# Kernel optimization log

Measured on AMD Instinct MI355X. Metric: run time of the kernel, lower is better.

Reference implementation:

```python
import jax, jax.numpy as jnp
import numpy as np

RADIUS = 1.0
NSAMPLE = 32


def _query_ball(new_xyz, xyz, radius, nsample):
    # new_xyz (B,M,3), xyz (B,N,3) -> idx (B,M,nsample) int32
    B, M, _ = new_xyz.shape
    N = xyz.shape[1]
    # squared distances via ||q||^2 + ||p||^2 - 2 q.p (avoids BxMxNx3 diff tensor)
    q2 = jnp.sum(new_xyz * new_xyz, axis=-1)          # (B,M)
    p2 = jnp.sum(xyz * xyz, axis=-1)                  # (B,N)
    qp = jnp.einsum('bmd,bnd->bmn', new_xyz, xyz)     # (B,M,N)
    dist2 = q2[:, :, None] + p2[:, None, :] - 2.0 * qp
    mask = dist2 < radius * radius
    ar = jnp.arange(N, dtype=jnp.int32)
    masked = jnp.where(mask, ar[None, None, :], jnp.int32(N + 1))  # (B,M,N)
    first = jnp.sort(masked, axis=2)[:, :, :nsample]               # (B,M,S)
    first_valid = first[:, :, :1]                                   # pad with first neighbor
    idx = jnp.where(first == N + 1, first_valid, first)
    return idx.astype(jnp.int32)


def _group(points, idx):
    # points (B,C,N), idx (B,M,S) -> (B,C,M,S) gather along N
    B, C, N = points.shape
    M, S = idx.shape[1], idx.shape[2]
    ie = jnp.broadcast_to(idx.reshape(B, 1, M * S).astype(jnp.int32), (B, C, M * S))
    return jnp.take_along_axis(points, ie, axis=2).reshape(B, C, M, S)


def setup_inputs() -> dict:
    key = jax.random.key(0)
    k1, k2 = jax.random.split(key)
    B, N, M, C = 8, 8192, 2048, 64
    xyz = jax.random.normal(k1, (B, N, 3), dtype=jnp.float32)
    # centroids are a subset of the cloud -> every ball query has >= 1 valid neighbor
    new_xyz = xyz[:, :M, :]
    features = jax.random.normal(k2, (B, C, N), dtype=jnp.float32)
    return {"xyz": xyz, "new_xyz": new_xyz, "features": features}


def reference(xyz, new_xyz, features):
    idx = _query_ball(new_xyz, xyz, RADIUS, NSAMPLE)                      # (B,M,S)
    grouped_xyz = _group(jnp.swapaxes(xyz, 1, 2), idx)                    # (B,3,M,S)
    grouped_xyz = grouped_xyz - jnp.swapaxes(new_xyz, 1, 2)[..., None]    # recenter
    grouped_feat = _group(features, idx)                                  # (B,C,M,S)
    return jnp.concatenate([grouped_xyz, grouped_feat], axis=1)           # (B,3+C,M,S)
```

## Files before the change

kernel.cpp:

```cpp
#include <hip/hip_runtime.h>

#define N_PTS 8192
#define M_Q   2048
#define C_F   64
#define NS    32
#define B_SZ  8


__global__ __launch_bounds__(256) void prep_kernel(
    const float* __restrict__ xyz, const float* __restrict__ nxyz,
    float4* __restrict__ xyz4, float* __restrict__ xyzT,
    float* __restrict__ nxyzT)
{
#pragma clang fp contract(off)
    const int i = blockIdx.x * 256 + (int)threadIdx.x;
    if (i < B_SZ * N_PTS) {
        const float p0 = xyz[i * 3 + 0];
        const float p1 = xyz[i * 3 + 1];
        const float p2 = xyz[i * 3 + 2];
        const float s  = (p0 * p0 + p1 * p1) + p2 * p2;
        xyz4[i] = make_float4(p0, p1, p2, s);
        const int b = i >> 13;
        const int n = i & (N_PTS - 1);
        xyzT[((size_t)b * 3 + 0) * N_PTS + n] = p0;
        xyzT[((size_t)b * 3 + 1) * N_PTS + n] = p1;
        xyzT[((size_t)b * 3 + 2) * N_PTS + n] = p2;
    } else {
        const int j = i - B_SZ * N_PTS;
        const float q0 = nxyz[j * 3 + 0];
        const float q1 = nxyz[j * 3 + 1];
        const float q2 = nxyz[j * 3 + 2];
        const int b = j >> 11;
        const int m = j & (M_Q - 1);
        nxyzT[((size_t)b * 3 + 0) * M_Q + m] = q0;
        nxyzT[((size_t)b * 3 + 1) * M_Q + m] = q1;
        nxyzT[((size_t)b * 3 + 2) * M_Q + m] = q2;
    }
}

__global__ __launch_bounds__(256) void scan_kernel(
    const float4* __restrict__ xyz4, const float* __restrict__ nxyz,
    int* __restrict__ gidx)
{
#pragma clang fp contract(off)
    const int lane = threadIdx.x & 63;
    const int w    = threadIdx.x >> 6;
    const int q    = blockIdx.x * 4 + w;
    const int b    = q >> 11;
    const float4* __restrict__ xb = xyz4 + (size_t)b * N_PTS;
    int* __restrict__ gout = gidx + (size_t)q * NS;

    const float* __restrict__ qp = nxyz + (size_t)q * 3;
    const float qx = qp[0], qy = qp[1], qz = qp[2];
    const float q2 = (qx * qx + qy * qy) + qz * qz;

    int  cnt = 0;
    int  first_idx = 0;
    bool have_first = false;

    for (int base = 0; base < N_PTS && cnt < NS; base += 256) {
        float4 P[4];
#pragma unroll
        for (int cc = 0; cc < 4; ++cc)
            P[cc] = xb[base + cc * 64 + lane];
#pragma unroll
        for (int cc = 0; cc < 4; ++cc) {
            if (cnt >= NS) break;
            const float qpdot = (qx * P[cc].x + qy * P[cc].y) + qz * P[cc].z;
            const float d2 = (q2 + P[cc].w) - 2.0f * qpdot;
            const bool pred = d2 < 1.0f;
            const unsigned long long mask = __ballot(pred);
            if (mask) {
                if (!have_first) {
                    first_idx = base + cc * 64 + __ffsll(mask) - 1;
                    have_first = true;
                }
                if (pred) {
                    const int pos = cnt + (int)__popcll(mask & ((1ull << lane) - 1ull));
                    if (pos < NS) gout[pos] = base + cc * 64 + lane;
                }
                cnt += (int)__popcll(mask);
            }
        }
    }
    if (cnt < NS) {
        for (int p = cnt + lane; p < NS; p += 64) gout[p] = first_idx;
    }
}

__global__ __launch_bounds__(256) void gather_kernel(
    const float* __restrict__ feat, const float* __restrict__ xyzT,
    const float* __restrict__ nxyzT, const int* __restrict__ gidx,
    float* __restrict__ out)
{
#pragma clang fp contract(off)
    __shared__ float plane[N_PTS];
    __shared__ float qsh[512];

    const int x   = blockIdx.x & 7;
    const int t   = blockIdx.x >> 3;
    const int gq  = t / 67;
    const int c   = t % 67;
    const int gid = gq * 8 + x;
    const int b   = gid >> 2;
    const int mq  = gid & 3;
    const int m0  = mq * 512;

    const float* __restrict__ src =
        (c < 3) ? (xyzT + ((size_t)b * 3 + c) * N_PTS)
                : (feat + ((size_t)b * C_F + (c - 3)) * N_PTS);

    {
        const float4* __restrict__ s4 = (const float4*)src;
        float4* p4 = (float4*)plane;
#pragma unroll
        for (int k = 0; k < 8; ++k)
            p4[k * 256 + threadIdx.x] = s4[k * 256 + threadIdx.x];
    }
    if (c < 3) {
        const float* __restrict__ qsrc = nxyzT + ((size_t)b * 3 + c) * M_Q + m0;
        qsh[threadIdx.x]       = qsrc[threadIdx.x];
        qsh[256 + threadIdx.x] = qsrc[256 + threadIdx.x];
    }
    __syncthreads();

    const int* __restrict__ idxp = gidx + ((size_t)b * M_Q + m0) * NS;
    float* __restrict__ op = out + (((size_t)b * 67 + c) * M_Q + m0) * NS;

    if (c < 3) {
#pragma unroll 4
        for (int it = 0; it < 16; ++it) {
            const int e  = it * 256 + (int)threadIdx.x;
            const int m  = e >> 3;
            const int s4 = (e & 7) * 4;
            const int4 nn = *(const int4*)(idxp + m * NS + s4);
            const float qc = qsh[m];
            float4 v;
            v.x = plane[nn.x] - qc;
            v.y = plane[nn.y] - qc;
            v.z = plane[nn.z] - qc;
            v.w = plane[nn.w] - qc;
            *(float4*)(op + (size_t)m * NS + s4) = v;
        }
    } else {
#pragma unroll 4
        for (int it = 0; it < 16; ++it) {
            const int e  = it * 256 + (int)threadIdx.x;
            const int m  = e >> 3;
            const int s4 = (e & 7) * 4;
            const int4 nn = *(const int4*)(idxp + m * NS + s4);
            float4 v;
            v.x = plane[nn.x];
            v.y = plane[nn.y];
            v.z = plane[nn.z];
            v.w = plane[nn.w];
            *(float4*)(op + (size_t)m * NS + s4) = v;
        }
    }
}

extern "C" void kernel_launch(void* const* d_in, const int* in_sizes, int n_in,
                              void* d_out, int out_size, void* d_ws, size_t ws_size,
                              hipStream_t stream)
{
    const float* xyz  = (const float*)d_in[0];
    const float* nxyz = (const float*)d_in[1];
    const float* feat = (const float*)d_in[2];
    float* out = (float*)d_out;

    float4* xyz4  = (float4*)d_ws;
    float*  xyzT  = (float*)((char*)d_ws + (2u << 20));
    float*  nxyzT = (float*)((char*)d_ws + (4u << 20));
    int*    gidx  = (int*)  ((char*)d_ws + (6u << 20));

    prep_kernel<<<(B_SZ * N_PTS + B_SZ * M_Q) / 256, 256, 0, stream>>>(
        xyz, nxyz, xyz4, xyzT, nxyzT);
    scan_kernel<<<(B_SZ * M_Q) / 4, 256, 0, stream>>>(xyz4, nxyz, gidx);
    gather_kernel<<<B_SZ * 67 * 4, 256, 0, stream>>>(feat, xyzT, nxyzT, gidx, out);
}
```

Before: 208.8 us.

## Drop transposed xyz copies, prefetch indices, use 512-thread gather with nontemporal stores

The prep kernel no longer writes transposed xyz and new_xyz planes. The gather kernel reads strided coordinates straight from the original arrays. The gather block grows to 512 threads and loads all neighbor indices into registers before the shared-memory plane fill, so index loads overlap the plane load. Output writes use nontemporal stores to avoid polluting the cache. In exchange, the xyz plane loads are strided and uncoalesced, and each thread holds more registers.

```diff
diff --git a/kernel.cpp b/kernel.cpp
--- a/kernel.cpp
+++ b/kernel.cpp
@@ -6,36 +6,19 @@
 #define NS    32
 #define B_SZ  8
 
+typedef float f32x4 __attribute__((ext_vector_type(4)));
+
 
 __global__ __launch_bounds__(256) void prep_kernel(
-    const float* __restrict__ xyz, const float* __restrict__ nxyz,
-    float4* __restrict__ xyz4, float* __restrict__ xyzT,
-    float* __restrict__ nxyzT)
+    const float* __restrict__ xyz, float4* __restrict__ xyz4)
 {
 #pragma clang fp contract(off)
     const int i = blockIdx.x * 256 + (int)threadIdx.x;
-    if (i < B_SZ * N_PTS) {
-        const float p0 = xyz[i * 3 + 0];
-        const float p1 = xyz[i * 3 + 1];
-        const float p2 = xyz[i * 3 + 2];
-        const float s  = (p0 * p0 + p1 * p1) + p2 * p2;
-        xyz4[i] = make_float4(p0, p1, p2, s);
-        const int b = i >> 13;
-        const int n = i & (N_PTS - 1);
-        xyzT[((size_t)b * 3 + 0) * N_PTS + n] = p0;
-        xyzT[((size_t)b * 3 + 1) * N_PTS + n] = p1;
-        xyzT[((size_t)b * 3 + 2) * N_PTS + n] = p2;
-    } else {
-        const int j = i - B_SZ * N_PTS;
-        const float q0 = nxyz[j * 3 + 0];
-        const float q1 = nxyz[j * 3 + 1];
-        const float q2 = nxyz[j * 3 + 2];
-        const int b = j >> 11;
-        const int m = j & (M_Q - 1);
-        nxyzT[((size_t)b * 3 + 0) * M_Q + m] = q0;
-        nxyzT[((size_t)b * 3 + 1) * M_Q + m] = q1;
-        nxyzT[((size_t)b * 3 + 2) * M_Q + m] = q2;
-    }
+    const float p0 = xyz[i * 3 + 0];
+    const float p1 = xyz[i * 3 + 1];
+    const float p2 = xyz[i * 3 + 2];
+    const float s  = (p0 * p0 + p1 * p1) + p2 * p2;
+    xyz4[i] = make_float4(p0, p1, p2, s);
 }
 
 __global__ __launch_bounds__(256) void scan_kernel(
@@ -88,15 +71,16 @@
     }
 }
 
-__global__ __launch_bounds__(256) void gather_kernel(
-    const float* __restrict__ feat, const float* __restrict__ xyzT,
-    const float* __restrict__ nxyzT, const int* __restrict__ gidx,
+__global__ __launch_bounds__(512) void gather_kernel(
+    const float* __restrict__ feat, const float* __restrict__ xyz,
+    const float* __restrict__ nxyz, const int* __restrict__ gidx,
     float* __restrict__ out)
 {
 #pragma clang fp contract(off)
     __shared__ float plane[N_PTS];
     __shared__ float qsh[512];
 
+    const int tid = (int)threadIdx.x;
     const int x   = blockIdx.x & 7;
     const int t   = blockIdx.x >> 3;
     const int gq  = t / 67;
@@ -106,55 +90,53 @@
     const int mq  = gid & 3;
     const int m0  = mq * 512;
 
-    const float* __restrict__ src =
-        (c < 3) ? (xyzT + ((size_t)b * 3 + c) * N_PTS)
-                : (feat + ((size_t)b * C_F + (c - 3)) * N_PTS);
+    const int* __restrict__ idxp = gidx + ((size_t)b * M_Q + m0) * NS;
+    int4 nn[8];
+#pragma unroll
+    for (int it = 0; it < 8; ++it)
+        nn[it] = *(const int4*)(idxp + (it * 512 + tid) * 4);
 
-    {
-        const float4* __restrict__ s4 = (const float4*)src;
+    if (c < 3) {
+        const float* __restrict__ src = xyz + (size_t)b * N_PTS * 3 + c;
+#pragma unroll
+        for (int k = 0; k < 16; ++k) {
+            const int n = k * 512 + tid;
+            plane[n] = src[(size_t)n * 3];
+        }
+        qsh[tid] = nxyz[((size_t)b * M_Q + m0 + tid) * 3 + c];
+    } else {
+        const float4* __restrict__ s4p =
+            (const float4*)(feat + ((size_t)b * C_F + (c - 3)) * N_PTS);
         float4* p4 = (float4*)plane;
 #pragma unroll
-        for (int k = 0; k < 8; ++k)
-            p4[k * 256 + threadIdx.x] = s4[k * 256 + threadIdx.x];
-    }
-    if (c < 3) {
-        const float* __restrict__ qsrc = nxyzT + ((size_t)b * 3 + c) * M_Q + m0;
-        qsh[threadIdx.x]       = qsrc[threadIdx.x];
-        qsh[256 + threadIdx.x] = qsrc[256 + threadIdx.x];
+        for (int k = 0; k < 4; ++k)
+            p4[k * 512 + tid] = s4p[k * 512 + tid];
     }
     __syncthreads();
 
-    const int* __restrict__ idxp = gidx + ((size_t)b * M_Q + m0) * NS;
     float* __restrict__ op = out + (((size_t)b * 67 + c) * M_Q + m0) * NS;
-
     if (c < 3) {
-#pragma unroll 4
-        for (int it = 0; it < 16; ++it) {
-            const int e  = it * 256 + (int)threadIdx.x;
-            const int m  = e >> 3;
-            const int s4 = (e & 7) * 4;
-            const int4 nn = *(const int4*)(idxp + m * NS + s4);
-            const float qc = qsh[m];
-            float4 v;
-            v.x = plane[nn.x] - qc;
-            v.y = plane[nn.y] - qc;
-            v.z = plane[nn.z] - qc;
-            v.w = plane[nn.w] - qc;
-            *(float4*)(op + (size_t)m * NS + s4) = v;
+#pragma unroll
+        for (int it = 0; it < 8; ++it) {
+            const int e  = it * 512 + tid;
+            const float qc = qsh[e >> 3];
+            f32x4 v;
+            v.x = plane[nn[it].x] - qc;
+            v.y = plane[nn[it].y] - qc;
+            v.z = plane[nn[it].z] - qc;
+            v.w = plane[nn[it].w] - qc;
+            __builtin_nontemporal_store(v, (f32x4*)(op + (size_t)e * 4));
         }
     } else {
-#pragma unroll 4
-        for (int it = 0; it < 16; ++it) {
-            const int e  = it * 256 + (int)threadIdx.x;
-            const int m  = e >> 3;
-            const int s4 = (e & 7) * 4;
-            const int4 nn = *(const int4*)(idxp + m * NS + s4);
-            float4 v;
-            v.x = plane[nn.x];
-            v.y = plane[nn.y];
-            v.z = plane[nn.z];
-            v.w = plane[nn.w];
-            *(float4*)(op + (size_t)m * NS + s4) = v;
+#pragma unroll
+        for (int it = 0; it < 8; ++it) {
+            const int e = it * 512 + tid;
+            f32x4 v;
+            v.x = plane[nn[it].x];
+            v.y = plane[nn[it].y];
+            v.z = plane[nn[it].z];
+            v.w = plane[nn[it].w];
+            __builtin_nontemporal_store(v, (f32x4*)(op + (size_t)e * 4));
         }
     }
 }
@@ -168,13 +150,10 @@
     const float* feat = (const float*)d_in[2];
     float* out = (float*)d_out;
 
-    float4* xyz4  = (float4*)d_ws;
-    float*  xyzT  = (float*)((char*)d_ws + (2u << 20));
-    float*  nxyzT = (float*)((char*)d_ws + (4u << 20));
-    int*    gidx  = (int*)  ((char*)d_ws + (6u << 20));
+    float4* xyz4 = (float4*)d_ws;
+    int*    gidx = (int*)((char*)d_ws + (2u << 20));
 
-    prep_kernel<<<(B_SZ * N_PTS + B_SZ * M_Q) / 256, 256, 0, stream>>>(
-        xyz, nxyz, xyz4, xyzT, nxyzT);
+    prep_kernel<<<(B_SZ * N_PTS) / 256, 256, 0, stream>>>(xyz, xyz4);
     scan_kernel<<<(B_SZ * M_Q) / 4, 256, 0, stream>>>(xyz4, nxyz, gidx);
-    gather_kernel<<<B_SZ * 67 * 4, 256, 0, stream>>>(feat, xyzT, nxyzT, gidx, out);
+    gather_kernel<<<B_SZ * 67 * 4, 512, 0, stream>>>(feat, xyz, nxyz, gidx, out);
 }
```

After: 191.0 us. 8.5% less time.
